# Optimization experiments

Hardware: AMD Instinct MI355X
Metric: run time of the kernel (lower is better)

Reference implementation:

```python
import jax, jax.numpy as jnp
import numpy as np

B = 128           # persons in batch
V = 128           # visits per person
CPV = 16          # codes per visit
MAX_VISITS = 510  # 512 - 2, hard-coded in module
D = 256           # embedding_dim * n_heads = 128 * 2
H = 2             # n_heads
DH = D // H
MAX_DAYS = 365
VOCAB = 30000
N_LAYERS = 2
DFF = 4 * D


def setup_inputs() -> dict:
    key = jax.random.key(0)
    ks = jax.random.split(key, 24)
    total_visits = B * V
    total_codes = total_visits * CPV
    all_codes = jax.random.randint(ks[0], (total_codes,), 0, VOCAB, dtype=jnp.int32)
    # code -> visit segment id (contiguous, as produced by the per-person loop)
    seg_ids = (jnp.arange(total_codes, dtype=jnp.int32) // CPV).astype(jnp.int32)
    # visit -> flattened slot in padded [B, MAX_VISITS] tensor (right-aligned)
    pos = MAX_VISITS - V + jnp.arange(V, dtype=jnp.int32)
    dest = (jnp.arange(B, dtype=jnp.int32)[:, None] * MAX_VISITS + pos[None, :]).reshape(-1)
    times = jax.random.uniform(ks[1], (total_visits,), minval=0.0, maxval=float(MAX_DAYS), dtype=jnp.float32)
    s = 0.02
    concept_emb = jax.random.normal(ks[2], (VOCAB, D), dtype=jnp.float32) * s
    pad_emb = jnp.zeros((D,), dtype=jnp.float32)
    Wq = jax.random.normal(ks[3], (N_LAYERS, D, D), dtype=jnp.float32) * s
    Wk = jax.random.normal(ks[4], (N_LAYERS, D, D), dtype=jnp.float32) * s
    Wv = jax.random.normal(ks[5], (N_LAYERS, D, D), dtype=jnp.float32) * s
    Wo = jax.random.normal(ks[6], (N_LAYERS, D, D), dtype=jnp.float32) * s
    W1 = jax.random.normal(ks[7], (N_LAYERS, D, DFF), dtype=jnp.float32) * s
    W2 = jax.random.normal(ks[8], (N_LAYERS, DFF, D), dtype=jnp.float32) * s
    z = lambda *sh: jnp.zeros(sh, dtype=jnp.float32)
    o = lambda *sh: jnp.ones(sh, dtype=jnp.float32)
    return dict(all_codes=all_codes, seg_ids=seg_ids, dest=dest, times=times,
                concept_emb=concept_emb, pad_emb=pad_emb,
                Wq=Wq, Wk=Wk, Wv=Wv, Wo=Wo,
                bq=z(N_LAYERS, D), bk=z(N_LAYERS, D), bv=z(N_LAYERS, D), bo=z(N_LAYERS, D),
                ln1_g=o(N_LAYERS, D), ln1_b=z(N_LAYERS, D),
                W1=W1, b1=z(N_LAYERS, DFF), W2=W2, b2=z(N_LAYERS, D),
                ln2_g=o(N_LAYERS, D), ln2_b=z(N_LAYERS, D))


def _ln(x, g, b):
    m = jnp.mean(x, axis=-1, keepdims=True)
    v = jnp.var(x, axis=-1, keepdims=True)
    return g * (x - m) * jax.lax.rsqrt(v + 1e-5) + b


def _forward(all_codes, seg_ids, dest, times, concept_emb, pad_emb,
             Wq, Wk, Wv, Wo, bq, bk, bv, bo, ln1_g, ln1_b,
             W1, b1, W2, b2, ln2_g, ln2_b):
    # gather code embeddings and segment-sum per visit (index_add_ in torch)
    emb = concept_emb[all_codes]                               # [total_codes, D]
    summed = jax.ops.segment_sum(emb, seg_ids, num_segments=B * V)  # [B*V, D]
    # scatter visits right-aligned into padded [B*MAX_VISITS, D], pad slots = pad_emb
    padded = jnp.broadcast_to(pad_emb, (B * MAX_VISITS, D)).at[dest].set(summed)
    # sinusoidal time embedding: timescales = ((1/1e4)**(1/D))**arange(D/2)
    t = jnp.clip(times, 0.0, float(MAX_DAYS - 1))
    ts = jnp.power(jnp.float32((1.0 / 10000.0) ** (1.0 / D)), jnp.arange(D // 2, dtype=jnp.float32))
    ang = t[:, None] * ts[None, :]                             # [B*V, D/2]
    te = jnp.concatenate([jnp.sin(ang), jnp.cos(ang)], axis=1) # [B*V, D]
    te_pad = jnp.zeros((B * MAX_VISITS, D), dtype=padded.dtype).at[dest].set(te)
    x = (padded + te_pad).reshape(B, MAX_VISITS, D)
    inv_sqrt_dh = np.float32(1.0 / np.sqrt(DH))
    for l in range(N_LAYERS):
        q = (x @ Wq[l] + bq[l]).reshape(B, MAX_VISITS, H, DH)
        k = (x @ Wk[l] + bk[l]).reshape(B, MAX_VISITS, H, DH)
        v = (x @ Wv[l] + bv[l]).reshape(B, MAX_VISITS, H, DH)
        scores = jnp.einsum('bqhd,bkhd->bhqk', q, k) * inv_sqrt_dh
        attn = jax.nn.softmax(scores, axis=-1)
        ctx = jnp.einsum('bhqk,bkhd->bqhd', attn, v).reshape(B, MAX_VISITS, D)
        x = _ln(x + ctx @ Wo[l] + bo[l], ln1_g[l], ln1_b[l])
        ff = jax.nn.relu(x @ W1[l] + b1[l]) @ W2[l] + b2[l]
        x = _ln(x + ff, ln2_g[l], ln2_b[l])
    return x


def reference(all_codes, seg_ids, dest, times, concept_emb, pad_emb,
              Wq, Wk, Wv, Wo, bq, bk, bv, bo, ln1_g, ln1_b,
              W1, b1, W2, b2, ln2_g, ln2_b):
    return _forward(all_codes, seg_ids, dest, times, concept_emb, pad_emb,
                    Wq, Wk, Wv, Wo, bq, bk, bv, bo, ln1_g, ln1_b,
                    W1, b1, W2, b2, ln2_g, ln2_b)
```

## Files before the change

### kernel.cpp

```cpp
#include <hip/hip_runtime.h>
#include <cstddef>

#define BATCH 128
#define NV 128
#define CPV 16
#define MAXV 510
#define NPAD 382
#define DIM 256
#define NH 2
#define DH 128
#define NLAYERS 2
#define DFF 1024
#define RROWS (BATCH * NV)
#define M2 (RROWS + BATCH)
#define AST 168
#define VST 160

typedef __attribute__((ext_vector_type(8))) short short8;
typedef __attribute__((ext_vector_type(4))) short short4v;
typedef __attribute__((ext_vector_type(4))) float floatx4;

__device__ __forceinline__ short f2bf(float f) {
    union { float f; unsigned u; } v; v.f = f;
    unsigned r = v.u + 0x7fffu + ((v.u >> 16) & 1u);
    return (short)(r >> 16);
}
__device__ __forceinline__ float bf2f(short s) {
    union { unsigned u; float f; } v; v.u = ((unsigned)(unsigned short)s) << 16;
    return v.f;
}

__device__ __forceinline__ void gload_lds16(const short* g, short* l) {
    __builtin_amdgcn_global_load_lds(
        (const __attribute__((address_space(1))) unsigned int*)g,
        (__attribute__((address_space(3))) unsigned int*)l,
        16, 0, 0);
}

__global__ __launch_bounds__(256) void wtrans_all(const float* __restrict__ Wq,
                                                  const float* __restrict__ Wk,
                                                  const float* __restrict__ Wv,
                                                  const float* __restrict__ Wo,
                                                  const float* __restrict__ W1,
                                                  const float* __restrict__ W2,
                                                  short* __restrict__ wqkvT,
                                                  short* __restrict__ woT,
                                                  short* __restrict__ w1T,
                                                  short* __restrict__ w2T) {
    int y = blockIdx.y;
    int l = y / 6, w = y - l * 6;
    const float* src; short* dst; int K, nsh;
    switch (w) {
        case 0:  src = Wq + (size_t)l * 65536;  dst = wqkvT + (size_t)l * 196608;           K = 256;  nsh = 8;  break;
        case 1:  src = Wk + (size_t)l * 65536;  dst = wqkvT + (size_t)l * 196608 + 65536;   K = 256;  nsh = 8;  break;
        case 2:  src = Wv + (size_t)l * 65536;  dst = wqkvT + (size_t)l * 196608 + 131072;  K = 256;  nsh = 8;  break;
        case 3:  src = Wo + (size_t)l * 65536;  dst = woT   + (size_t)l * 65536;            K = 256;  nsh = 8;  break;
        case 4:  src = W1 + (size_t)l * 262144; dst = w1T   + (size_t)l * 262144;           K = 256;  nsh = 10; break;
        default: src = W2 + (size_t)l * 262144; dst = w2T   + (size_t)l * 262144;           K = 1024; nsh = 8;  break;
    }
    int N = 1 << nsh;
    int idx = blockIdx.x * 256 + threadIdx.x;
    if (idx >= K * N) return;
    int k = idx >> nsh, n = idx & (N - 1);
    dst[(size_t)n * K + k] = f2bf(src[idx]);
}

__global__ __launch_bounds__(256) void build_x(const int* __restrict__ codes,
                                               const float* __restrict__ times,
                                               const float* __restrict__ cemb,
                                               const float* __restrict__ pemb,
                                               short* __restrict__ x) {
    int row = blockIdx.x;
    int d = threadIdx.x;
    float val;
    if (row >= RROWS) {
        val = pemb[d];
    } else {
        int b = row >> 7;
        int r = row & 127;
        int visit = b * NV + r;
        const int* cb = codes + visit * CPV;
        float s = 0.f;
#pragma unroll
        for (int c = 0; c < CPV; ++c)
            s += cemb[(size_t)cb[c] * DIM + d];
        float t = times[visit];
        t = fminf(fmaxf(t, 0.f), 364.f);
        int i = d & 127;
        float ang = t * expf(-0.03597789207803197f * (float)i);
        float te = (d < 128) ? sinf(ang) : cosf(ang);
        val = s + te;
    }
    x[(size_t)row * DIM + d] = f2bf(val);
}

__global__ __launch_bounds__(256) void gemm_qkv(const short* __restrict__ A,
                                                const short* __restrict__ BT,
                                                const float* __restrict__ bq,
                                                const float* __restrict__ bk,
                                                const float* __restrict__ bv,
                                                short* __restrict__ qo,
                                                short* __restrict__ ko,
                                                short* __restrict__ vo) {
    __shared__ __align__(16) short lA[2][128 * 32];
    __shared__ __align__(16) short lB[2][128 * 32];
    int tid = threadIdx.x;
    int wave = tid >> 6, lane = tid & 63;
    int l15 = lane & 15, quad = lane >> 4;
    int q8 = quad * 8;
    int m0 = blockIdx.y * 128;
    int n0 = blockIdx.x * 128;
    int sel = blockIdx.x >> 1;
    int nloc = n0 & 255;
    int wm = (wave & 1) * 64;
    int wn = (wave >> 1) * 64;

    int srow = tid >> 2;
    int skoff = (tid & 3) * 8;
    const short* ag = A + (size_t)(m0 + srow) * DIM + skoff;
    const short* bg = BT + (size_t)(n0 + srow) * DIM + skoff;
    const size_t rstep = (size_t)64 * DIM;
    int t8 = tid * 8;

    floatx4 acc[4][4];
#pragma unroll
    for (int i = 0; i < 4; ++i)
#pragma unroll
        for (int j = 0; j < 4; ++j) acc[i][j] = (floatx4){0.f, 0.f, 0.f, 0.f};

    gload_lds16(ag, lA[0] + t8);
    gload_lds16(ag + rstep, lA[0] + 2048 + t8);
    gload_lds16(bg, lB[0] + t8);
    gload_lds16(bg + rstep, lB[0] + 2048 + t8);
    __syncthreads();
    int cur = 0;
#pragma unroll
    for (int k0 = 0; k0 < 8; ++k0) {
        if (k0 < 7) {
            int kn = (k0 + 1) * 32;
            gload_lds16(ag + kn, lA[cur ^ 1] + t8);
            gload_lds16(ag + rstep + kn, lA[cur ^ 1] + 2048 + t8);
            gload_lds16(bg + kn, lB[cur ^ 1] + t8);
            gload_lds16(bg + rstep + kn, lB[cur ^ 1] + 2048 + t8);
        }
        short8 aF[4], bF[4];
#pragma unroll
        for (int t = 0; t < 4; ++t) {
            aF[t] = *(const short8*)(lA[cur] + (wm + t * 16 + l15) * 32 + q8);
            bF[t] = *(const short8*)(lB[cur] + (wn + t * 16 + l15) * 32 + q8);
        }
#pragma unroll
        for (int i = 0; i < 4; ++i)
#pragma unroll
            for (int j = 0; j < 4; ++j)
                acc[i][j] = __builtin_amdgcn_mfma_f32_16x16x32_bf16(aF[i], bF[j], acc[i][j], 0, 0, 0);
        __syncthreads();
        cur ^= 1;
    }

    const float* bias = (sel == 0) ? bq : (sel == 1) ? bk : bv;
    short* out = (sel == 0) ? qo : (sel == 1) ? ko : vo;
#pragma unroll
    for (int j = 0; j < 4; ++j) {
        int col = nloc + wn + j * 16 + l15;
        float bval = bias[col];
#pragma unroll
        for (int i = 0; i < 4; ++i) {
#pragma unroll
            for (int r = 0; r < 4; ++r) {
                int row = m0 + wm + i * 16 + quad * 4 + r;
                out[(size_t)row * DIM + col] = f2bf(acc[i][j][r] + bval);
            }
        }
    }
}

__global__ __launch_bounds__(256) void gemm_wo_ln(const short* __restrict__ CTX,
                                                  const short* __restrict__ WoT,
                                                  const float* __restrict__ bo,
                                                  const short* __restrict__ X,
                                                  const float* __restrict__ g,
                                                  const float* __restrict__ bta,
                                                  short* __restrict__ xout) {
    __shared__ __align__(16) short lA[2][64 * 32];
    __shared__ __align__(16) short lB[2][256 * 32];
    int tid = threadIdx.x;
    int wave = tid >> 6, lane = tid & 63;
    int l15 = lane & 15, quad = lane >> 4;
    int q8 = quad * 8;
    int m0 = blockIdx.x * 64;
    int wr = wave * 16;
    int srow = tid >> 2;
    int skoff = (tid & 3) * 8;
    const short* ag = CTX + (size_t)(m0 + srow) * DIM + skoff;
    const short* bg = WoT + (size_t)srow * DIM + skoff;
    int t8 = tid * 8;

    floatx4 acc[16];
#pragma unroll
    for (int j = 0; j < 16; ++j) acc[j] = (floatx4){0.f, 0.f, 0.f, 0.f};

    gload_lds16(ag, lA[0] + t8);
    gload_lds16(bg, lB[0] + t8);
    gload_lds16(bg + (size_t)64 * DIM, lB[0] + 2048 + t8);
    gload_lds16(bg + (size_t)128 * DIM, lB[0] + 4096 + t8);
    gload_lds16(bg + (size_t)192 * DIM, lB[0] + 6144 + t8);
    __syncthreads();
    int cur = 0;
#pragma unroll
    for (int k0 = 0; k0 < 8; ++k0) {
        if (k0 < 7) {
            int kn = (k0 + 1) * 32;
            gload_lds16(ag + kn, lA[cur ^ 1] + t8);
            gload_lds16(bg + kn, lB[cur ^ 1] + t8);
            gload_lds16(bg + (size_t)64 * DIM + kn, lB[cur ^ 1] + 2048 + t8);
            gload_lds16(bg + (size_t)128 * DIM + kn, lB[cur ^ 1] + 4096 + t8);
            gload_lds16(bg + (size_t)192 * DIM + kn, lB[cur ^ 1] + 6144 + t8);
        }
        short8 aF = *(const short8*)(lA[cur] + (wr + l15) * 32 + q8);
#pragma unroll
        for (int j = 0; j < 16; ++j) {
            short8 bF = *(const short8*)(lB[cur] + (j * 16 + l15) * 32 + q8);
            acc[j] = __builtin_amdgcn_mfma_f32_16x16x32_bf16(aF, bF, acc[j], 0, 0, 0);
        }
        __syncthreads();
        cur ^= 1;
    }

    float bias[16], gam[16], bet[16];
#pragma unroll
    for (int j = 0; j < 16; ++j) {
        int col = j * 16 + l15;
        bias[j] = bo[col]; gam[j] = g[col]; bet[j] = bta[col];
    }
#pragma unroll
    for (int r = 0; r < 4; ++r) {
        int row = m0 + wr + quad * 4 + r;
        float v[16], s = 0.f, sq = 0.f;
#pragma unroll
        for (int j = 0; j < 16; ++j) {
            v[j] = acc[j][r] + bias[j] + bf2f(X[(size_t)row * DIM + j * 16 + l15]);
            s += v[j]; sq += v[j] * v[j];
        }
        s += __shfl_xor(s, 1); sq += __shfl_xor(sq, 1);
        s += __shfl_xor(s, 2); sq += __shfl_xor(sq, 2);
        s += __shfl_xor(s, 4); sq += __shfl_xor(sq, 4);
        s += __shfl_xor(s, 8); sq += __shfl_xor(sq, 8);
        float mean = s * (1.f / 256.f);
        float var = fmaxf(sq * (1.f / 256.f) - mean * mean, 0.f);
        float rstd = rsqrtf(var + 1e-5f);
#pragma unroll
        for (int j = 0; j < 16; ++j) {
            float y = gam[j] * (v[j] - mean) * rstd + bet[j];
            xout[(size_t)row * DIM + j * 16 + l15] = f2bf(y);
        }
    }
}

#define PST 136
__global__ __launch_bounds__(256, 2) void ff_fused(const short* __restrict__ X,
                                                   const short* __restrict__ W1T,
                                                   const float* __restrict__ b1,
                                                   const short* __restrict__ W2T,
                                                   const float* __restrict__ b2,
                                                   const float* __restrict__ g2,
                                                   const float* __restrict__ bt2,
                                                   short* __restrict__ xout,
                                                   float* __restrict__ fout,
                                                   float* __restrict__ padrowF) {
    __shared__ __align__(16) short lA[2][64 * 32];
    __shared__ __align__(16) short lB[2][128 * 32];
    __shared__ __align__(16) short lB2[2][256 * 32];
    __shared__ __align__(16) short lP[64 * PST];
    __shared__ float redS[4][32], redQ[4][32];
    int tid = threadIdx.x;
    int wave = tid >> 6, lane = tid & 63;
    int l15 = lane & 15, quad = lane >> 4;
    int q8 = quad * 8;
    int m0 = blockIdx.x * 64;
    int wm = (wave & 1) * 32;
    int wf = (wave >> 1) * 64;
    int wn2 = (wave >> 1) * 128;
    int srow = tid >> 2;
    int spart = (tid & 3) * 8;
    const short* xg = X + (size_t)(m0 + srow) * DIM + spart;
    int t8 = tid * 8;

    floatx4 acc2[2][8];
#pragma unroll
    for (int i = 0; i < 2; ++i)
#pragma unroll
        for (int j = 0; j < 8; ++j) acc2[i][j] = (floatx4){0.f, 0.f, 0.f, 0.f};

    for (int f0 = 0; f0 < DFF; f0 += 128) {
        const short* w1g = W1T + (size_t)(f0 + srow) * DIM + spart;
        floatx4 acc1[2][4];
#pragma unroll
        for (int i = 0; i < 2; ++i)
#pragma unroll
            for (int j = 0; j < 4; ++j) acc1[i][j] = (floatx4){0.f, 0.f, 0.f, 0.f};

        gload_lds16(xg, lA[0] + t8);
        gload_lds16(w1g, lB[0] + t8);
        gload_lds16(w1g + (size_t)64 * DIM, lB[0] + 2048 + t8);
        __syncthreads();
        int cur = 0;
#pragma unroll
        for (int k0 = 0; k0 < 8; ++k0) {
            if (k0 < 7) {
                int kn = (k0 + 1) * 32;
                gload_lds16(xg + kn, lA[cur ^ 1] + t8);
                gload_lds16(w1g + kn, lB[cur ^ 1] + t8);
                gload_lds16(w1g + (size_t)64 * DIM + kn, lB[cur ^ 1] + 2048 + t8);
            }
            short8 aF[2], bF[4];
#pragma unroll
            for (int t = 0; t < 2; ++t)
                aF[t] = *(const short8*)(lA[cur] + (wm + t * 16 + l15) * 32 + q8);
#pragma unroll
            for (int t = 0; t < 4; ++t)
                bF[t] = *(const short8*)(lB[cur] + (wf + t * 16 + l15) * 32 + q8);
#pragma unroll
            for (int i = 0; i < 2; ++i)
#pragma unroll
                for (int j = 0; j < 4; ++j)
                    acc1[i][j] = __builtin_amdgcn_mfma_f32_16x16x32_bf16(aF[i], bF[j], acc1[i][j], 0, 0, 0);
            __syncthreads();
            cur ^= 1;
        }

        {
            const short* w2g = W2T + (size_t)srow * DFF + f0 + spart;
            gload_lds16(w2g, lB2[0] + t8);
            gload_lds16(w2g + (size_t)64 * DFF, lB2[0] + 2048 + t8);
            gload_lds16(w2g + (size_t)128 * DFF, lB2[0] + 4096 + t8);
            gload_lds16(w2g + (size_t)192 * DFF, lB2[0] + 6144 + t8);
        }
#pragma unroll
        for (int j = 0; j < 4; ++j) {
            int fc = wf + j * 16 + l15;
            float bval = b1[f0 + fc];
#pragma unroll
            for (int i = 0; i < 2; ++i) {
#pragma unroll
                for (int r = 0; r < 4; ++r) {
                    float v = acc1[i][j][r] + bval;
                    lP[(wm + i * 16 + quad * 4 + r) * PST + fc] = f2bf(fmaxf(v, 0.f));
                }
            }
        }
        __syncthreads();
        cur = 0;
#pragma unroll
        for (int ks = 0; ks < 4; ++ks) {
            if (ks < 3) {
                const short* w2g = W2T + (size_t)srow * DFF + f0 + (ks + 1) * 32 + spart;
                gload_lds16(w2g, lB2[cur ^ 1] + t8);
                gload_lds16(w2g + (size_t)64 * DFF, lB2[cur ^ 1] + 2048 + t8);
                gload_lds16(w2g + (size_t)128 * DFF, lB2[cur ^ 1] + 4096 + t8);
                gload_lds16(w2g + (size_t)192 * DFF, lB2[cur ^ 1] + 6144 + t8);
            }
            short8 aP[2], bW[8];
#pragma unroll
            for (int t = 0; t < 2; ++t)
                aP[t] = *(const short8*)(lP + (wm + t * 16 + l15) * PST + ks * 32 + q8);
#pragma unroll
            for (int j = 0; j < 8; ++j)
                bW[j] = *(const short8*)(lB2[cur] + (wn2 + j * 16 + l15) * 32 + q8);
#pragma unroll
            for (int i = 0; i < 2; ++i)
#pragma unroll
                for (int j = 0; j < 8; ++j)
                    acc2[i][j] = __builtin_amdgcn_mfma_f32_16x16x32_bf16(aP[i], bW[j], acc2[i][j], 0, 0, 0);
            __syncthreads();
            cur ^= 1;
        }
    }

    float b2v[8];
#pragma unroll
    for (int j = 0; j < 8; ++j) b2v[j] = b2[wn2 + j * 16 + l15];
#pragma unroll
    for (int i = 0; i < 2; ++i) {
#pragma unroll
        for (int r = 0; r < 4; ++r) {
            int row = m0 + wm + i * 16 + quad * 4 + r;
            float s = 0.f, sq = 0.f;
#pragma unroll
            for (int j = 0; j < 8; ++j) {
                float v = acc2[i][j][r] + b2v[j] + bf2f(X[(size_t)row * DIM + wn2 + j * 16 + l15]);
                acc2[i][j][r] = v;
                s += v; sq += v * v;
            }
            s += __shfl_xor(s, 1); sq += __shfl_xor(sq, 1);
            s += __shfl_xor(s, 2); sq += __shfl_xor(sq, 2);
            s += __shfl_xor(s, 4); sq += __shfl_xor(sq, 4);
            s += __shfl_xor(s, 8); sq += __shfl_xor(sq, 8);
            if (l15 == 0) {
                int idx = i * 16 + quad * 4 + r;
                redS[wave][idx] = s;
                redQ[wave][idx] = sq;
            }
        }
    }
    __syncthreads();
    float gam[8], bet[8];
#pragma unroll
    for (int j = 0; j < 8; ++j) {
        int col = wn2 + j * 16 + l15;
        gam[j] = g2[col]; bet[j] = bt2[col];
    }
#pragma unroll
    for (int i = 0; i < 2; ++i) {
#pragma unroll
        for (int r = 0; r < 4; ++r) {
            int idx = i * 16 + quad * 4 + r;
            float ts = redS[wave][idx] + redS[wave ^ 2][idx];
            float tq = redQ[wave][idx] + redQ[wave ^ 2][idx];
            float mean = ts * (1.f / 256.f);
            float var = fmaxf(tq * (1.f / 256.f) - mean * mean, 0.f);
            float rstd = rsqrtf(var + 1e-5f);
            int grow = m0 + wm + i * 16 + quad * 4 + r;
            if (!fout) {
#pragma unroll
                for (int j = 0; j < 8; ++j) {
                    float y = gam[j] * (acc2[i][j][r] - mean) * rstd + bet[j];
                    xout[(size_t)grow * DIM + wn2 + j * 16 + l15] = f2bf(y);
                }
            } else if (grow < RROWS) {
                int bb = grow >> 7, rr = grow & 127;
                float* dst = fout + ((size_t)bb * MAXV + NPAD + rr) * DIM;
#pragma unroll
                for (int j = 0; j < 8; ++j) {
                    float y = gam[j] * (acc2[i][j][r] - mean) * rstd + bet[j];
                    dst[wn2 + j * 16 + l15] = y;
                }
            } else {
                float* dst = padrowF + (size_t)(grow - RROWS) * DIM;
#pragma unroll
                for (int j = 0; j < 8; ++j) {
                    float y = gam[j] * (acc2[i][j][r] - mean) * rstd + bet[j];
                    dst[wn2 + j * 16 + l15] = y;
                }
            }
        }
    }
}

__global__ __launch_bounds__(256) void pad_attn(const short* __restrict__ q,
                                                const short* __restrict__ k,
                                                const short* __restrict__ v,
                                                short* __restrict__ ctx) {
    __shared__ float qv[256], wgt[2][128], wp[2], den[2];
    int b = blockIdx.x, tid = threadIdx.x;
    int h = tid >> 7, kk = tid & 127;
    const float scale = 0.08838834764831845f;
    qv[tid] = bf2f(q[(size_t)(RROWS + b) * DIM + tid]);
    __syncthreads();
    {
        const short8* krow = (const short8*)(k + (size_t)(b * NV + kk) * DIM + h * DH);
        float s = 0.f;
#pragma unroll
        for (int c = 0; c < 16; ++c) {
            short8 k8 = krow[c];
#pragma unroll
            for (int e = 0; e < 8; ++e) s += bf2f(k8[e]) * qv[h * DH + c * 8 + e];
        }
        wgt[h][kk] = __expf(fminf(s * scale, 30.f));
    }
    if (kk == 0) {
        const short8* kp = (const short8*)(k + (size_t)(RROWS + b) * DIM + h * DH);
        float sp = 0.f;
#pragma unroll
        for (int c = 0; c < 16; ++c) {
            short8 k8 = kp[c];
#pragma unroll
            for (int e = 0; e < 8; ++e) sp += bf2f(k8[e]) * qv[h * DH + c * 8 + e];
        }
        wp[h] = 382.f * __expf(fminf(sp * scale, 30.f));
    }
    __syncthreads();
    if (kk == 0) {
        float d = wp[h];
        for (int i = 0; i < 128; ++i) d += wgt[h][i];
        den[h] = d;
    }
    __syncthreads();
    {
        const short* vcol = v + (size_t)(b * NV) * DIM + h * DH + kk;
        float c = 0.f;
#pragma unroll 8
        for (int key = 0; key < 128; ++key) c += wgt[h][key] * bf2f(vcol[(size_t)key * DIM]);
        c += wp[h] * bf2f(v[(size_t)(RROWS + b) * DIM + h * DH + kk]);
        ctx[(size_t)(RROWS + b) * DIM + tid] = f2bf(c / den[h]);
    }
}

__global__ __launch_bounds__(256) void pad_bcast(const float* __restrict__ padrow,
                                                 float* __restrict__ fout) {
    int b = blockIdx.y;
    int p = blockIdx.x * 4 + (threadIdx.x >> 6);
    if (p >= NPAD) return;
    int d4 = (threadIdx.x & 63) * 4;
    floatx4 v = *(const floatx4*)(padrow + (size_t)b * DIM + d4);
    *(floatx4*)(fout + ((size_t)b * MAXV + p) * DIM + d4) = v;
}

__global__ __launch_bounds__(256) void transpose_v(const short* __restrict__ v,
                                                   short* __restrict__ vT) {
    __shared__ short lds[32][33];
    int pair = blockIdx.y;
    int b = pair >> 1, h = pair & 1;
    int st = blockIdx.x % 5;
    int dt = blockIdx.x / 5;
    int tid = threadIdx.x;
    int sl = tid >> 3, dl = (tid & 7) * 4;
    short4v val;
    if (st < 4) {
        const short* src = v + ((size_t)(b * NV + st * 32 + sl)) * DIM + h * DH + dt * 32 + dl;
        val = *(const short4v*)src;
    } else {
        val = (short4v){0, 0, 0, 0};
        if (sl == 0)
            val = *(const short4v*)(v + (size_t)(RROWS + b) * DIM + h * DH + dt * 32 + dl);
    }
#pragma unroll
    for (int j = 0; j < 4; ++j) lds[sl][dl + j] = val[j];
    __syncthreads();
    int drow = tid >> 3, scol = (tid & 7) * 4;
    short* dst = vT + (size_t)pair * DH * VST + (size_t)(dt * 32 + drow) * VST + st * 32 + scol;
#pragma unroll
    for (int j = 0; j < 4; ++j) dst[j] = lds[scol + j][drow];
}

__global__ __launch_bounds__(256) void attn_fused(const short* __restrict__ q,
                                                  const short* __restrict__ k,
                                                  const short* __restrict__ vT,
                                                  short* __restrict__ ctx) {
    __shared__ __align__(16) short lA[64 * 32];
    __shared__ __align__(16) short lB[128 * 32];
    __shared__ __align__(16) short lS[64 * AST];
    int tid = threadIdx.x;
    int wave = tid >> 6, lane = tid & 63;
    int l15 = lane & 15, quad = lane >> 4;
    int q8 = quad * 8;
    int pair = blockIdx.y;
    int b = pair >> 1, h = pair & 1;
    int m0 = blockIdx.x * 64;
    int wm = (wave & 1) * 32;
    int wn = (wave >> 1) * 64;

    int srow = tid >> 2;
    int skoff = (tid & 3) * 8;
    const short* ag = q + (size_t)(b * NV + m0 + srow) * DIM + h * DH + skoff;
    const short* bg = k + (size_t)(b * NV + srow) * DIM + h * DH + skoff;
    const short* kp = k + (size_t)(RROWS + b) * DIM + h * DH + q8;
    short* lA_dst = lA + tid * 8;
    short* lB_dst = lB + tid * 8;
    const float scale = 0.08838834764831845f;

    {
        int zr = tid >> 2, zc = 144 + (tid & 3) * 4;
        *(short4v*)(lS + zr * AST + zc) = (short4v){0, 0, 0, 0};
    }

    floatx4 sacc[2][4];
    floatx4 sacct[2];
#pragma unroll
    for (int i = 0; i < 2; ++i) {
#pragma unroll
        for (int j = 0; j < 4; ++j) sacc[i][j] = (floatx4){0.f, 0.f, 0.f, 0.f};
        sacct[i] = (floatx4){0.f, 0.f, 0.f, 0.f};
    }

#pragma unroll
    for (int k0 = 0; k0 < DH; k0 += 32) {
        gload_lds16(ag + k0, lA_dst);
        gload_lds16(bg + k0, lB_dst);
        gload_lds16(bg + (size_t)64 * DIM + k0, lB_dst + 2048);
        __syncthreads();
        short8 aF[2], bF[4];
#pragma unroll
        for (int t = 0; t < 2; ++t)
            aF[t] = *(const short8*)(lA + (wm + t * 16 + l15) * 32 + q8);
#pragma unroll
        for (int t = 0; t < 4; ++t)
            bF[t] = *(const short8*)(lB + (wn + t * 16 + l15) * 32 + q8);
#pragma unroll
        for (int i = 0; i < 2; ++i)
#pragma unroll
            for (int j = 0; j < 4; ++j)
                sacc[i][j] = __builtin_amdgcn_mfma_f32_16x16x32_bf16(aF[i], bF[j], sacc[i][j], 0, 0, 0);
        if (wn == 0) {
            short8 bFt = (l15 == 0) ? *(const short8*)(kp + k0) : (short8){0,0,0,0,0,0,0,0};
#pragma unroll
            for (int i = 0; i < 2; ++i)
                sacct[i] = __builtin_amdgcn_mfma_f32_16x16x32_bf16(aF[i], bFt, sacct[i], 0, 0, 0);
        }
        __syncthreads();
    }
#pragma unroll
    for (int j = 0; j < 4; ++j) {
        int col = wn + j * 16 + l15;
#pragma unroll
        for (int i = 0; i < 2; ++i) {
#pragma unroll
            for (int r = 0; r < 4; ++r) {
                lS[(wm + i * 16 + quad * 4 + r) * AST + col] =
                    f2bf(__expf(fminf(sacc[i][j][r] * scale, 30.f)));
            }
        }
    }
    if (wn == 0) {
        float wt = (l15 == 0) ? 382.f : 0.f;
#pragma unroll
        for (int i = 0; i < 2; ++i) {
#pragma unroll
            for (int r = 0; r < 4; ++r) {
                lS[(wm + i * 16 + quad * 4 + r) * AST + 128 + l15] =
                    f2bf(wt * __expf(fminf(sacct[i][r] * scale, 30.f)));
            }
        }
    }
    __syncthreads();
    const short* vg = vT + (size_t)pair * DH * VST + (size_t)srow * VST + skoff;
    floatx4 oacc[2][4];
#pragma unroll
    for (int i = 0; i < 2; ++i)
#pragma unroll
        for (int j = 0; j < 4; ++j) oacc[i][j] = (floatx4){0.f, 0.f, 0.f, 0.f};
    float rsum[2] = {0.f, 0.f};

#pragma unroll
    for (int ks = 0; ks < 5; ++ks) {
        gload_lds16(vg + ks * 32, lB_dst);
        gload_lds16(vg + (size_t)64 * VST + ks * 32, lB_dst + 2048);
        __syncthreads();
        short8 aP[2], bV[4];
#pragma unroll
        for (int t = 0; t < 2; ++t)
            aP[t] = *(const short8*)(lS + (wm + t * 16 + l15) * AST + ks * 32 + q8);
#pragma unroll
        for (int t = 0; t < 4; ++t)
            bV[t] = *(const short8*)(lB + (wn + t * 16 + l15) * 32 + q8);
#pragma unroll
        for (int i = 0; i < 2; ++i) {
            float s = 0.f;
#pragma unroll
            for (int e = 0; e < 8; ++e) s += bf2f(aP[i][e]);
            rsum[i] += s;
        }
#pragma unroll
        for (int i = 0; i < 2; ++i)
#pragma unroll
            for (int j = 0; j < 4; ++j)
                oacc[i][j] = __builtin_amdgcn_mfma_f32_16x16x32_bf16(aP[i], bV[j], oacc[i][j], 0, 0, 0);
        __syncthreads();
    }

#pragma unroll
    for (int i = 0; i < 2; ++i) {
        rsum[i] += __shfl_xor(rsum[i], 16);
        rsum[i] += __shfl_xor(rsum[i], 32);
    }
    short* outb = ctx + (size_t)(b * NV + m0) * DIM + h * DH;
#pragma unroll
    for (int i = 0; i < 2; ++i) {
#pragma unroll
        for (int r = 0; r < 4; ++r) {
            float inv = 1.f / __shfl(rsum[i], quad * 4 + r);
#pragma unroll
            for (int j = 0; j < 4; ++j) {
                int col = wn + j * 16 + l15;
                int row = wm + i * 16 + quad * 4 + r;
                outb[(size_t)row * DIM + col] = f2bf(oacc[i][j][r] * inv);
            }
        }
    }
}

extern "C" void kernel_launch(void* const* d_in, const int* in_sizes, int n_in,
                              void* d_out, int out_size, void* d_ws, size_t ws_size,
                              hipStream_t stream) {
    const int*   all_codes = (const int*)d_in[0];
    const float* times = (const float*)d_in[3];
    const float* cemb  = (const float*)d_in[4];
    const float* pemb  = (const float*)d_in[5];
    const float* Wq = (const float*)d_in[6];
    const float* Wk = (const float*)d_in[7];
    const float* Wv = (const float*)d_in[8];
    const float* Wo = (const float*)d_in[9];
    const float* bq = (const float*)d_in[10];
    const float* bk = (const float*)d_in[11];
    const float* bv = (const float*)d_in[12];
    const float* bo = (const float*)d_in[13];
    const float* ln1g = (const float*)d_in[14];
    const float* ln1b = (const float*)d_in[15];
    const float* W1 = (const float*)d_in[16];
    const float* b1 = (const float*)d_in[17];
    const float* W2 = (const float*)d_in[18];
    const float* b2 = (const float*)d_in[19];
    const float* ln2g = (const float*)d_in[20];
    const float* ln2b = (const float*)d_in[21];

    char* ws = (char*)d_ws;
    short* wqkvT = (short*)ws;
    short* woT   = wqkvT + 2 * 196608;
    short* w1T   = woT + 2 * 65536;
    short* w2T   = w1T + 2 * 262144;
    float* padrowF = (float*)(ws + (3500u << 10));

    const size_t SLOT = (size_t)M2 * DIM;
    short* xb = (short*)(ws + (4u << 20));
    short* C0 = xb + SLOT;
    short* C1 = C0 + SLOT;
    short* C2 = C1 + SLOT;
    short* C3 = C2 + SLOT;
    short* C4 = C3 + SLOT;

    wtrans_all<<<dim3(1024, 12), 256, 0, stream>>>(Wq, Wk, Wv, Wo, W1, W2,
                                                   wqkvT, woT, w1T, w2T);
    build_x<<<M2, 256, 0, stream>>>(all_codes, times, cemb, pemb, xb);

    for (int l = 0; l < NLAYERS; ++l) {
        const short* qkv_l = wqkvT + (size_t)l * 196608;
        const short* wo_l = woT + (size_t)l * 65536;
        const short* w1_l = w1T + (size_t)l * 262144;
        const short* w2_l = w2T + (size_t)l * 262144;
        int last = (l == NLAYERS - 1);

        gemm_qkv<<<dim3(6, M2 / 128), 256, 0, stream>>>(xb, qkv_l, bq + l * 256, bk + l * 256,
                                                        bv + l * 256, C0, C1, C2);
        transpose_v<<<dim3(20, BATCH * NH), 256, 0, stream>>>(C2, C4);
        attn_fused<<<dim3(2, BATCH * NH), 256, 0, stream>>>(C0, C1, C4, C3);
        pad_attn<<<BATCH, 256, 0, stream>>>(C0, C1, C2, C3);
        gemm_wo_ln<<<M2 / 64, 256, 0, stream>>>(C3, wo_l, bo + l * 256, xb,
                                                ln1g + l * 256, ln1b + l * 256, C0);
        ff_fused<<<M2 / 64, 256, 0, stream>>>(C0, w1_l, b1 + l * 1024, w2_l, b2 + l * 256,
                                              ln2g + l * 256, ln2b + l * 256, xb,
                                              last ? (float*)d_out : nullptr,
                                              last ? padrowF : nullptr);
        if (last)
            pad_bcast<<<dim3(96, BATCH), 256, 0, stream>>>(padrowF, (float*)d_out);
    }
}
```

Measured before the change: 415.7 us.

## Halve row tile in Wo+LN and fused FFN kernels to double block count

Shrinks the M tile of gemm_wo_ln and ff_fused from 64 to 32 rows, so twice as many blocks launch (M2/32, about 516). In gemm_wo_ln the four waves now split the 256 output columns two ways, which needs a cross-wave LayerNorm reduction through shared memory plus an extra barrier. The aim is better CU occupancy and load balance across the many compute units, since 258 blocks underfill the GPU. In exchange, weight tiles (W1, W2, Wo) are reloaded from L2 twice as often per row, and each wave has fewer MFMAs per LDS load.

```diff
diff --git a/kernel.cpp b/kernel.cpp
--- a/kernel.cpp
+++ b/kernel.cpp
@@ -182,25 +182,27 @@
                                                   const float* __restrict__ g,
                                                   const float* __restrict__ bta,
                                                   short* __restrict__ xout) {
-    __shared__ __align__(16) short lA[2][64 * 32];
+    __shared__ __align__(16) short lA[2][32 * 32];
     __shared__ __align__(16) short lB[2][256 * 32];
+    __shared__ float redS[4][16], redQ[4][16];
     int tid = threadIdx.x;
     int wave = tid >> 6, lane = tid & 63;
     int l15 = lane & 15, quad = lane >> 4;
     int q8 = quad * 8;
-    int m0 = blockIdx.x * 64;
-    int wr = wave * 16;
-    int srow = tid >> 2;
+    int m0 = blockIdx.x * 32;
+    int wm = (wave & 1) * 16;
+    int wn = (wave >> 1) * 128;
+    int arow = tid >> 2;
     int skoff = (tid & 3) * 8;
-    const short* ag = CTX + (size_t)(m0 + srow) * DIM + skoff;
-    const short* bg = WoT + (size_t)srow * DIM + skoff;
+    const short* ag = CTX + (size_t)(m0 + (arow & 31)) * DIM + skoff;
+    const short* bg = WoT + (size_t)arow * DIM + skoff;
     int t8 = tid * 8;
 
-    floatx4 acc[16];
-#pragma unroll
-    for (int j = 0; j < 16; ++j) acc[j] = (floatx4){0.f, 0.f, 0.f, 0.f};
-
-    gload_lds16(ag, lA[0] + t8);
+    floatx4 acc[8];
+#pragma unroll
+    for (int j = 0; j < 8; ++j) acc[j] = (floatx4){0.f, 0.f, 0.f, 0.f};
+
+    if (wave < 2) gload_lds16(ag, lA[0] + t8);
     gload_lds16(bg, lB[0] + t8);
     gload_lds16(bg + (size_t)64 * DIM, lB[0] + 2048 + t8);
     gload_lds16(bg + (size_t)128 * DIM, lB[0] + 4096 + t8);
@@ -211,48 +213,61 @@
     for (int k0 = 0; k0 < 8; ++k0) {
         if (k0 < 7) {
             int kn = (k0 + 1) * 32;
-            gload_lds16(ag + kn, lA[cur ^ 1] + t8);
+            if (wave < 2) gload_lds16(ag + kn, lA[cur ^ 1] + t8);
             gload_lds16(bg + kn, lB[cur ^ 1] + t8);
             gload_lds16(bg + (size_t)64 * DIM + kn, lB[cur ^ 1] + 2048 + t8);
             gload_lds16(bg + (size_t)128 * DIM + kn, lB[cur ^ 1] + 4096 + t8);
             gload_lds16(bg + (size_t)192 * DIM + kn, lB[cur ^ 1] + 6144 + t8);
         }
-        short8 aF = *(const short8*)(lA[cur] + (wr + l15) * 32 + q8);
-#pragma unroll
-        for (int j = 0; j < 16; ++j) {
-            short8 bF = *(const short8*)(lB[cur] + (j * 16 + l15) * 32 + q8);
+        short8 aF = *(const short8*)(lA[cur] + (wm + l15) * 32 + q8);
+#pragma unroll
+        for (int j = 0; j < 8; ++j) {
+            short8 bF = *(const short8*)(lB[cur] + (wn + j * 16 + l15) * 32 + q8);
             acc[j] = __builtin_amdgcn_mfma_f32_16x16x32_bf16(aF, bF, acc[j], 0, 0, 0);
         }
         __syncthreads();
         cur ^= 1;
     }
 
-    float bias[16], gam[16], bet[16];
-#pragma unroll
-    for (int j = 0; j < 16; ++j) {
-        int col = j * 16 + l15;
+    float bias[8], gam[8], bet[8];
+#pragma unroll
+    for (int j = 0; j < 8; ++j) {
+        int col = wn + j * 16 + l15;
         bias[j] = bo[col]; gam[j] = g[col]; bet[j] = bta[col];
     }
+    float v[4][8];
 #pragma unroll
     for (int r = 0; r < 4; ++r) {
-        int row = m0 + wr + quad * 4 + r;
-        float v[16], s = 0.f, sq = 0.f;
-#pragma unroll
-        for (int j = 0; j < 16; ++j) {
-            v[j] = acc[j][r] + bias[j] + bf2f(X[(size_t)row * DIM + j * 16 + l15]);
-            s += v[j]; sq += v[j] * v[j];
+        int row = m0 + wm + quad * 4 + r;
+        float s = 0.f, sq = 0.f;
+#pragma unroll
+        for (int j = 0; j < 8; ++j) {
+            v[r][j] = acc[j][r] + bias[j] + bf2f(X[(size_t)row * DIM + wn + j * 16 + l15]);
+            s += v[r][j]; sq += v[r][j] * v[r][j];
         }
         s += __shfl_xor(s, 1); sq += __shfl_xor(sq, 1);
         s += __shfl_xor(s, 2); sq += __shfl_xor(sq, 2);
         s += __shfl_xor(s, 4); sq += __shfl_xor(sq, 4);
         s += __shfl_xor(s, 8); sq += __shfl_xor(sq, 8);
-        float mean = s * (1.f / 256.f);
-        float var = fmaxf(sq * (1.f / 256.f) - mean * mean, 0.f);
+        if (l15 == 0) {
+            redS[wave][quad * 4 + r] = s;
+            redQ[wave][quad * 4 + r] = sq;
+        }
+    }
+    __syncthreads();
+#pragma unroll
+    for (int r = 0; r < 4; ++r) {
+        int idx = quad * 4 + r;
+        float ts = redS[wave][idx] + redS[wave ^ 2][idx];
+        float tq = redQ[wave][idx] + redQ[wave ^ 2][idx];
+        float mean = ts * (1.f / 256.f);
+        float var = fmaxf(tq * (1.f / 256.f) - mean * mean, 0.f);
         float rstd = rsqrtf(var + 1e-5f);
-#pragma unroll
-        for (int j = 0; j < 16; ++j) {
-            float y = gam[j] * (v[j] - mean) * rstd + bet[j];
-            xout[(size_t)row * DIM + j * 16 + l15] = f2bf(y);
+        int row = m0 + wm + quad * 4 + r;
+#pragma unroll
+        for (int j = 0; j < 8; ++j) {
+            float y = gam[j] * (v[r][j] - mean) * rstd + bet[j];
+            xout[(size_t)row * DIM + wn + j * 16 + l15] = f2bf(y);
         }
     }
 }
@@ -268,39 +283,35 @@
                                                    short* __restrict__ xout,
                                                    float* __restrict__ fout,
                                                    float* __restrict__ padrowF) {
-    __shared__ __align__(16) short lA[2][64 * 32];
+    __shared__ __align__(16) short lA[2][32 * 32];
     __shared__ __align__(16) short lB[2][128 * 32];
     __shared__ __align__(16) short lB2[2][256 * 32];
-    __shared__ __align__(16) short lP[64 * PST];
-    __shared__ float redS[4][32], redQ[4][32];
+    __shared__ __align__(16) short lP[32 * PST];
+    __shared__ float redS[4][16], redQ[4][16];
     int tid = threadIdx.x;
     int wave = tid >> 6, lane = tid & 63;
     int l15 = lane & 15, quad = lane >> 4;
     int q8 = quad * 8;
-    int m0 = blockIdx.x * 64;
-    int wm = (wave & 1) * 32;
+    int m0 = blockIdx.x * 32;
+    int wm = (wave & 1) * 16;
     int wf = (wave >> 1) * 64;
     int wn2 = (wave >> 1) * 128;
-    int srow = tid >> 2;
+    int arow = tid >> 2;
     int spart = (tid & 3) * 8;
-    const short* xg = X + (size_t)(m0 + srow) * DIM + spart;
+    const short* xg = X + (size_t)(m0 + (arow & 31)) * DIM + spart;
     int t8 = tid * 8;
 
-    floatx4 acc2[2][8];
-#pragma unroll
-    for (int i = 0; i < 2; ++i)
-#pragma unroll
-        for (int j = 0; j < 8; ++j) acc2[i][j] = (floatx4){0.f, 0.f, 0.f, 0.f};
+    floatx4 acc2[8];
+#pragma unroll
+    for (int j = 0; j < 8; ++j) acc2[j] = (floatx4){0.f, 0.f, 0.f, 0.f};
 
     for (int f0 = 0; f0 < DFF; f0 += 128) {
-        const short* w1g = W1T + (size_t)(f0 + srow) * DIM + spart;
-        floatx4 acc1[2][4];
-#pragma unroll
-        for (int i = 0; i < 2; ++i)
-#pragma unroll
-            for (int j = 0; j < 4; ++j) acc1[i][j] = (floatx4){0.f, 0.f, 0.f, 0.f};
-
-        gload_lds16(xg, lA[0] + t8);
+        const short* w1g = W1T + (size_t)(f0 + arow) * DIM + spart;
+        floatx4 acc1[4];
+#pragma unroll
+        for (int j = 0; j < 4; ++j) acc1[j] = (floatx4){0.f, 0.f, 0.f, 0.f};
+
+        if (wave < 2) gload_lds16(xg, lA[0] + t8);
         gload_lds16(w1g, lB[0] + t8);
         gload_lds16(w1g + (size_t)64 * DIM, lB[0] + 2048 + t8);
         __syncthreads();
@@ -309,28 +320,24 @@
         for (int k0 = 0; k0 < 8; ++k0) {
             if (k0 < 7) {
                 int kn = (k0 + 1) * 32;
-                gload_lds16(xg + kn, lA[cur ^ 1] + t8);
+                if (wave < 2) gload_lds16(xg + kn, lA[cur ^ 1] + t8);
                 gload_lds16(w1g + kn, lB[cur ^ 1] + t8);
                 gload_lds16(w1g + (size_t)64 * DIM + kn, lB[cur ^ 1] + 2048 + t8);
             }
-            short8 aF[2], bF[4];
-#pragma unroll
-            for (int t = 0; t < 2; ++t)
-                aF[t] = *(const short8*)(lA[cur] + (wm + t * 16 + l15) * 32 + q8);
+            short8 aF = *(const short8*)(lA[cur] + (wm + l15) * 32 + q8);
+            short8 bF[4];
 #pragma unroll
             for (int t = 0; t < 4; ++t)
                 bF[t] = *(const short8*)(lB[cur] + (wf + t * 16 + l15) * 32 + q8);
 #pragma unroll
-            for (int i = 0; i < 2; ++i)
-#pragma unroll
-                for (int j = 0; j < 4; ++j)
-                    acc1[i][j] = __builtin_amdgcn_mfma_f32_16x16x32_bf16(aF[i], bF[j], acc1[i][j], 0, 0, 0);
+            for (int j = 0; j < 4; ++j)
+                acc1[j] = __builtin_amdgcn_mfma_f32_16x16x32_bf16(aF, bF[j], acc1[j], 0, 0, 0);
             __syncthreads();
             cur ^= 1;
         }
 
         {
-            const short* w2g = W2T + (size_t)srow * DFF + f0 + spart;
+            const short* w2g = W2T + (size_t)arow * DFF + f0 + spart;
             gload_lds16(w2g, lB2[0] + t8);
             gload_lds16(w2g + (size_t)64 * DFF, lB2[0] + 2048 + t8);
             gload_lds16(w2g + (size_t)128 * DFF, lB2[0] + 4096 + t8);
@@ -341,12 +348,9 @@
             int fc = wf + j * 16 + l15;
             float bval = b1[f0 + fc];
 #pragma unroll
-            for (int i = 0; i < 2; ++i) {
-#pragma unroll
-                for (int r = 0; r < 4; ++r) {
-                    float v = acc1[i][j][r] + bval;
-                    lP[(wm + i * 16 + quad * 4 + r) * PST + fc] = f2bf(fmaxf(v, 0.f));
-                }
+            for (int r = 0; r < 4; ++r) {
+                float v = acc1[j][r] + bval;
+                lP[(wm + quad * 4 + r) * PST + fc] = f2bf(fmaxf(v, 0.f));
             }
         }
         __syncthreads();
@@ -354,24 +358,20 @@
 #pragma unroll
         for (int ks = 0; ks < 4; ++ks) {
             if (ks < 3) {
-                const short* w2g = W2T + (size_t)srow * DFF + f0 + (ks + 1) * 32 + spart;
+                const short* w2g = W2T + (size_t)arow * DFF + f0 + (ks + 1) * 32 + spart;
                 gload_lds16(w2g, lB2[cur ^ 1] + t8);
                 gload_lds16(w2g + (size_t)64 * DFF, lB2[cur ^ 1] + 2048 + t8);
                 gload_lds16(w2g + (size_t)128 * DFF, lB2[cur ^ 1] + 4096 + t8);
                 gload_lds16(w2g + (size_t)192 * DFF, lB2[cur ^ 1] + 6144 + t8);
             }
-            short8 aP[2], bW[8];
-#pragma unroll
-            for (int t = 0; t < 2; ++t)
-                aP[t] = *(const short8*)(lP + (wm + t * 16 + l15) * PST + ks * 32 + q8);
+            short8 aP = *(const short8*)(lP + (wm + l15) * PST + ks * 32 + q8);
+            short8 bW[8];
 #pragma unroll
             for (int j = 0; j < 8; ++j)
                 bW[j] = *(const short8*)(lB2[cur] + (wn2 + j * 16 + l15) * 32 + q8);
 #pragma unroll
-            for (int i = 0; i < 2; ++i)
-#pragma unroll
-                for (int j = 0; j < 8; ++j)
-                    acc2[i][j] = __builtin_amdgcn_mfma_f32_16x16x32_bf16(aP[i], bW[j], acc2[i][j], 0, 0, 0);
+            for (int j = 0; j < 8; ++j)
+                acc2[j] = __builtin_amdgcn_mfma_f32_16x16x32_bf16(aP, bW[j], acc2[j], 0, 0, 0);
             __syncthreads();
             cur ^= 1;
         }
@@ -380,27 +380,23 @@
     float b2v[8];
 #pragma unroll
     for (int j = 0; j < 8; ++j) b2v[j] = b2[wn2 + j * 16 + l15];
-#pragma unroll
-    for (int i = 0; i < 2; ++i) {
-#pragma unroll
-        for (int r = 0; r < 4; ++r) {
-            int row = m0 + wm + i * 16 + quad * 4 + r;
-            float s = 0.f, sq = 0.f;
-#pragma unroll
-            for (int j = 0; j < 8; ++j) {
-                float v = acc2[i][j][r] + b2v[j] + bf2f(X[(size_t)row * DIM + wn2 + j * 16 + l15]);
-                acc2[i][j][r] = v;
-                s += v; sq += v * v;
-            }
-            s += __shfl_xor(s, 1); sq += __shfl_xor(sq, 1);
-            s += __shfl_xor(s, 2); sq += __shfl_xor(sq, 2);
-            s += __shfl_xor(s, 4); sq += __shfl_xor(sq, 4);
-            s += __shfl_xor(s, 8); sq += __shfl_xor(sq, 8);
-            if (l15 == 0) {
-                int idx = i * 16 + quad * 4 + r;
-                redS[wave][idx] = s;
-                redQ[wave][idx] = sq;
-            }
+    float v[4][8];
+#pragma unroll
+    for (int r = 0; r < 4; ++r) {
+        int row = m0 + wm + quad * 4 + r;
+        float s = 0.f, sq = 0.f;
+#pragma unroll
+        for (int j = 0; j < 8; ++j) {
+            v[r][j] = acc2[j][r] + b2v[j] + bf2f(X[(size_t)row * DIM + wn2 + j * 16 + l15]);
+            s += v[r][j]; sq += v[r][j] * v[r][j];
+        }
+        s += __shfl_xor(s, 1); sq += __shfl_xor(sq, 1);
+        s += __shfl_xor(s, 2); sq += __shfl_xor(sq, 2);
+        s += __shfl_xor(s, 4); sq += __shfl_xor(sq, 4);
+        s += __shfl_xor(s, 8); sq += __shfl_xor(sq, 8);
+        if (l15 == 0) {
+            redS[wave][quad * 4 + r] = s;
+            redQ[wave][quad * 4 + r] = sq;
         }
     }
     __syncthreads();
@@ -411,37 +407,34 @@
         gam[j] = g2[col]; bet[j] = bt2[col];
     }
 #pragma unroll
-    for (int i = 0; i < 2; ++i) {
-#pragma unroll
-        for (int r = 0; r < 4; ++r) {
-            int idx = i * 16 + quad * 4 + r;
-            float ts = redS[wave][idx] + redS[wave ^ 2][idx];
-            float tq = redQ[wave][idx] + redQ[wave ^ 2][idx];
-            float mean = ts * (1.f / 256.f);
-            float var = fmaxf(tq * (1.f / 256.f) - mean * mean, 0.f);
-            float rstd = rsqrtf(var + 1e-5f);
-            int grow = m0 + wm + i * 16 + quad * 4 + r;
-            if (!fout) {
-#pragma unroll
-                for (int j = 0; j < 8; ++j) {
-                    float y = gam[j] * (acc2[i][j][r] - mean) * rstd + bet[j];
-                    xout[(size_t)grow * DIM + wn2 + j * 16 + l15] = f2bf(y);
-                }
-            } else if (grow < RROWS) {
-                int bb = grow >> 7, rr = grow & 127;
-                float* dst = fout + ((size_t)bb * MAXV + NPAD + rr) * DIM;
-#pragma unroll
-                for (int j = 0; j < 8; ++j) {
-                    float y = gam[j] * (acc2[i][j][r] - mean) * rstd + bet[j];
-                    dst[wn2 + j * 16 + l15] = y;
-                }
-            } else {
-                float* dst = padrowF + (size_t)(grow - RROWS) * DIM;
-#pragma unroll
-                for (int j = 0; j < 8; ++j) {
-                    float y = gam[j] * (acc2[i][j][r] - mean) * rstd + bet[j];
-                    dst[wn2 + j * 16 + l15] = y;
-                }
+    for (int r = 0; r < 4; ++r) {
+        int idx = quad * 4 + r;
+        float ts = redS[wave][idx] + redS[wave ^ 2][idx];
+        float tq = redQ[wave][idx] + redQ[wave ^ 2][idx];
+        float mean = ts * (1.f / 256.f);
+        float var = fmaxf(tq * (1.f / 256.f) - mean * mean, 0.f);
+        float rstd = rsqrtf(var + 1e-5f);
+        int grow = m0 + wm + quad * 4 + r;
+        if (!fout) {
+#pragma unroll
+            for (int j = 0; j < 8; ++j) {
+                float y = gam[j] * (v[r][j] - mean) * rstd + bet[j];
+                xout[(size_t)grow * DIM + wn2 + j * 16 + l15] = f2bf(y);
+            }
+        } else if (grow < RROWS) {
+            int bb = grow >> 7, rr = grow & 127;
+            float* dst = fout + ((size_t)bb * MAXV + NPAD + rr) * DIM;
+#pragma unroll
+            for (int j = 0; j < 8; ++j) {
+                float y = gam[j] * (v[r][j] - mean) * rstd + bet[j];
+                dst[wn2 + j * 16 + l15] = y;
+            }
+        } else {
+            float* dst = padrowF + (size_t)(grow - RROWS) * DIM;
+#pragma unroll
+            for (int j = 0; j < 8; ++j) {
+                float y = gam[j] * (v[r][j] - mean) * rstd + bet[j];
+                dst[wn2 + j * 16 + l15] = y;
             }
         }
     }
@@ -734,9 +727,9 @@
         transpose_v<<<dim3(20, BATCH * NH), 256, 0, stream>>>(C2, C4);
         attn_fused<<<dim3(2, BATCH * NH), 256, 0, stream>>>(C0, C1, C4, C3);
         pad_attn<<<BATCH, 256, 0, stream>>>(C0, C1, C2, C3);
-        gemm_wo_ln<<<M2 / 64, 256, 0, stream>>>(C3, wo_l, bo + l * 256, xb,
+        gemm_wo_ln<<<M2 / 32, 256, 0, stream>>>(C3, wo_l, bo + l * 256, xb,
                                                 ln1g + l * 256, ln1b + l * 256, C0);
-        ff_fused<<<M2 / 64, 256, 0, stream>>>(C0, w1_l, b1 + l * 1024, w2_l, b2 + l * 256,
+        ff_fused<<<M2 / 32, 256, 0, stream>>>(C0, w1_l, b1 + l * 1024, w2_l, b2 + l * 256,
                                               ln2g + l * 256, ln2b + l * 256, xb,
                                               last ? (float*)d_out : nullptr,
                                               last ? padrowF : nullptr);
```

Result: slower. 466.0 us (+12.1%).

## Split fused FFN over the hidden dimension and move LayerNorm to a separate kernel

Applied to the files above, without the earlier changes.

The fused FFN kernel is split in two. The FFN GEMMs now run on a 2D grid where each block handles half of the 1024-wide hidden dimension and writes an fp32 partial output. A new per-row kernel sums the two partials, adds the bias and residual, and applies LayerNorm. The goal is to double the number of blocks for the FFN, since M2/64 = 258 blocks may underfill the GPU. The cost is an extra fp32 partial write and read round trip (about 34 MB) plus one more kernel launch.

```diff
diff --git a/kernel.cpp b/kernel.cpp
--- a/kernel.cpp
+++ b/kernel.cpp
@@ -258,26 +258,22 @@
 }
 
 #define PST 136
-__global__ __launch_bounds__(256, 2) void ff_fused(const short* __restrict__ X,
-                                                   const short* __restrict__ W1T,
-                                                   const float* __restrict__ b1,
-                                                   const short* __restrict__ W2T,
-                                                   const float* __restrict__ b2,
-                                                   const float* __restrict__ g2,
-                                                   const float* __restrict__ bt2,
-                                                   short* __restrict__ xout,
-                                                   float* __restrict__ fout,
-                                                   float* __restrict__ padrowF) {
+__global__ __launch_bounds__(256, 2) void ff_part(const short* __restrict__ X,
+                                                  const short* __restrict__ W1T,
+                                                  const float* __restrict__ b1,
+                                                  const short* __restrict__ W2T,
+                                                  float* __restrict__ P0,
+                                                  float* __restrict__ P1) {
     __shared__ __align__(16) short lA[2][64 * 32];
     __shared__ __align__(16) short lB[2][128 * 32];
     __shared__ __align__(16) short lB2[2][256 * 32];
     __shared__ __align__(16) short lP[64 * PST];
-    __shared__ float redS[4][32], redQ[4][32];
     int tid = threadIdx.x;
     int wave = tid >> 6, lane = tid & 63;
     int l15 = lane & 15, quad = lane >> 4;
     int q8 = quad * 8;
     int m0 = blockIdx.x * 64;
+    int half = blockIdx.y;
     int wm = (wave & 1) * 32;
     int wf = (wave >> 1) * 64;
     int wn2 = (wave >> 1) * 128;
@@ -292,7 +288,8 @@
 #pragma unroll
         for (int j = 0; j < 8; ++j) acc2[i][j] = (floatx4){0.f, 0.f, 0.f, 0.f};
 
-    for (int f0 = 0; f0 < DFF; f0 += 128) {
+    int fbeg = half * 512;
+    for (int f0 = fbeg; f0 < fbeg + 512; f0 += 128) {
         const short* w1g = W1T + (size_t)(f0 + srow) * DIM + spart;
         floatx4 acc1[2][4];
 #pragma unroll
@@ -377,73 +374,55 @@
         }
     }
 
-    float b2v[8];
-#pragma unroll
-    for (int j = 0; j < 8; ++j) b2v[j] = b2[wn2 + j * 16 + l15];
+    float* Pp = half ? P1 : P0;
 #pragma unroll
     for (int i = 0; i < 2; ++i) {
 #pragma unroll
         for (int r = 0; r < 4; ++r) {
             int row = m0 + wm + i * 16 + quad * 4 + r;
-            float s = 0.f, sq = 0.f;
-#pragma unroll
-            for (int j = 0; j < 8; ++j) {
-                float v = acc2[i][j][r] + b2v[j] + bf2f(X[(size_t)row * DIM + wn2 + j * 16 + l15]);
-                acc2[i][j][r] = v;
-                s += v; sq += v * v;
-            }
-            s += __shfl_xor(s, 1); sq += __shfl_xor(sq, 1);
-            s += __shfl_xor(s, 2); sq += __shfl_xor(sq, 2);
-            s += __shfl_xor(s, 4); sq += __shfl_xor(sq, 4);
-            s += __shfl_xor(s, 8); sq += __shfl_xor(sq, 8);
-            if (l15 == 0) {
-                int idx = i * 16 + quad * 4 + r;
-                redS[wave][idx] = s;
-                redQ[wave][idx] = sq;
-            }
-        }
-    }
+#pragma unroll
+            for (int j = 0; j < 8; ++j)
+                Pp[(size_t)row * DIM + wn2 + j * 16 + l15] = acc2[i][j][r];
+        }
+    }
+}
+
+__global__ __launch_bounds__(256) void ff_ln2(const float* __restrict__ P0,
+                                              const float* __restrict__ P1,
+                                              const float* __restrict__ b2,
+                                              const short* __restrict__ X,
+                                              const float* __restrict__ g2,
+                                              const float* __restrict__ bt2,
+                                              short* __restrict__ xout,
+                                              float* __restrict__ fout,
+                                              float* __restrict__ padrowF) {
+    __shared__ float red[4][2];
+    int row = blockIdx.x;
+    int d = threadIdx.x;
+    float v = P0[(size_t)row * DIM + d] + P1[(size_t)row * DIM + d] + b2[d]
+            + bf2f(X[(size_t)row * DIM + d]);
+    float s = v, sq = v * v;
+#pragma unroll
+    for (int off = 1; off < 64; off <<= 1) {
+        s += __shfl_xor(s, off);
+        sq += __shfl_xor(sq, off);
+    }
+    int wave = threadIdx.x >> 6, lane = threadIdx.x & 63;
+    if (lane == 0) { red[wave][0] = s; red[wave][1] = sq; }
     __syncthreads();
-    float gam[8], bet[8];
-#pragma unroll
-    for (int j = 0; j < 8; ++j) {
-        int col = wn2 + j * 16 + l15;
-        gam[j] = g2[col]; bet[j] = bt2[col];
-    }
-#pragma unroll
-    for (int i = 0; i < 2; ++i) {
-#pragma unroll
-        for (int r = 0; r < 4; ++r) {
-            int idx = i * 16 + quad * 4 + r;
-            float ts = redS[wave][idx] + redS[wave ^ 2][idx];
-            float tq = redQ[wave][idx] + redQ[wave ^ 2][idx];
-            float mean = ts * (1.f / 256.f);
-            float var = fmaxf(tq * (1.f / 256.f) - mean * mean, 0.f);
-            float rstd = rsqrtf(var + 1e-5f);
-            int grow = m0 + wm + i * 16 + quad * 4 + r;
-            if (!fout) {
-#pragma unroll
-                for (int j = 0; j < 8; ++j) {
-                    float y = gam[j] * (acc2[i][j][r] - mean) * rstd + bet[j];
-                    xout[(size_t)grow * DIM + wn2 + j * 16 + l15] = f2bf(y);
-                }
-            } else if (grow < RROWS) {
-                int bb = grow >> 7, rr = grow & 127;
-                float* dst = fout + ((size_t)bb * MAXV + NPAD + rr) * DIM;
-#pragma unroll
-                for (int j = 0; j < 8; ++j) {
-                    float y = gam[j] * (acc2[i][j][r] - mean) * rstd + bet[j];
-                    dst[wn2 + j * 16 + l15] = y;
-                }
-            } else {
-                float* dst = padrowF + (size_t)(grow - RROWS) * DIM;
-#pragma unroll
-                for (int j = 0; j < 8; ++j) {
-                    float y = gam[j] * (acc2[i][j][r] - mean) * rstd + bet[j];
-                    dst[wn2 + j * 16 + l15] = y;
-                }
-            }
-        }
+    float ts = red[0][0] + red[1][0] + red[2][0] + red[3][0];
+    float tq = red[0][1] + red[1][1] + red[2][1] + red[3][1];
+    float mean = ts * (1.f / 256.f);
+    float var = fmaxf(tq * (1.f / 256.f) - mean * mean, 0.f);
+    float rstd = rsqrtf(var + 1e-5f);
+    float y = g2[d] * (v - mean) * rstd + bt2[d];
+    if (!fout) {
+        xout[(size_t)row * DIM + d] = f2bf(y);
+    } else if (row < RROWS) {
+        int bb = row >> 7, rr = row & 127;
+        fout[((size_t)bb * MAXV + NPAD + rr) * DIM + d] = y;
+    } else {
+        padrowF[(size_t)(row - RROWS) * DIM + d] = y;
     }
 }
 
@@ -717,6 +696,8 @@
     short* C2 = C1 + SLOT;
     short* C3 = C2 + SLOT;
     short* C4 = C3 + SLOT;
+    float* P0 = (float*)(C4 + (size_t)256 * 128 * VST);
+    float* P1 = P0 + (size_t)M2 * DIM;
 
     wtrans_all<<<dim3(1024, 12), 256, 0, stream>>>(Wq, Wk, Wv, Wo, W1, W2,
                                                    wqkvT, woT, w1T, w2T);
@@ -736,10 +717,11 @@
         pad_attn<<<BATCH, 256, 0, stream>>>(C0, C1, C2, C3);
         gemm_wo_ln<<<M2 / 64, 256, 0, stream>>>(C3, wo_l, bo + l * 256, xb,
                                                 ln1g + l * 256, ln1b + l * 256, C0);
-        ff_fused<<<M2 / 64, 256, 0, stream>>>(C0, w1_l, b1 + l * 1024, w2_l, b2 + l * 256,
-                                              ln2g + l * 256, ln2b + l * 256, xb,
-                                              last ? (float*)d_out : nullptr,
-                                              last ? padrowF : nullptr);
+        ff_part<<<dim3(M2 / 64, 2), 256, 0, stream>>>(C0, w1_l, b1 + l * 1024, w2_l, P0, P1);
+        ff_ln2<<<M2, 256, 0, stream>>>(P0, P1, b2 + l * 256, C0,
+                                       ln2g + l * 256, ln2b + l * 256, xb,
+                                       last ? (float*)d_out : nullptr,
+                                       last ? padrowF : nullptr);
         if (last)
             pad_bcast<<<dim3(96, BATCH), 256, 0, stream>>>(padrowF, (float*)d_out);
     }
```

After: 443.4 us. 6.7% more time.
